# Kernel tuning notes

Hardware: AMD Instinct MI355X
Metric: run time of the kernel (lower is better)

## Reference

```python
import jax, jax.numpy as jnp
import numpy as np

D = 1024   # hidden_dim
F = 4096   # ffn_dim
E = 8      # expert_num
K = 2      # top_k
B, S = 2, 2048

def setup_inputs() -> dict:
    key = jax.random.key(0)
    ks = jax.random.split(key, 5)
    scale = 0.02
    x = jax.random.normal(ks[0], (B, S, D), dtype=jnp.float32)
    gate_w = jax.random.normal(ks[1], (D, E), dtype=jnp.float32) * scale
    w1 = jax.random.normal(ks[2], (E, D, F), dtype=jnp.float32) * scale
    w3 = jax.random.normal(ks[3], (E, D, F), dtype=jnp.float32) * scale
    w2 = jax.random.normal(ks[4], (E, F, D), dtype=jnp.float32) * scale
    return {"x": x, "gate_w": gate_w, "w1": w1, "w3": w3, "w2": w2}

def reference(x, gate_w, w1, w3, w2):
    # x: [B, S, D] -> tokens [T, D]
    Bb, Ss, Dd = x.shape
    xt = x.reshape(-1, Dd)                                  # [T, D]
    T = xt.shape[0]
    # Router: softmax over experts in float32 (matches torch dtype=torch.float)
    router_probs = jax.nn.softmax((xt @ gate_w).astype(jnp.float32), axis=-1)  # [T, E]
    topk_w, topk_idx = jax.lax.top_k(router_probs, K)        # [T, K]
    topk_w = topk_w / topk_w.sum(axis=-1, keepdims=True)
    topk_w = topk_w.astype(x.dtype)
    # Combine weights scattered to dense [T, E] (equivalent to per-expert gather/scatter loop)
    combine = jnp.zeros((T, E), dtype=x.dtype).at[jnp.arange(T)[:, None], topk_idx].add(topk_w)
    # SwishFFN per expert: w2(silu(x w1) * (x w3)), no bias
    h = jax.nn.silu(jnp.einsum('td,edf->etf', xt, w1)) * jnp.einsum('td,edf->etf', xt, w3)  # [E, T, F]
    out_e = jnp.einsum('etf,efd->etd', h, w2)                # [E, T, D]
    out = jnp.einsum('etd,te->td', out_e, combine)           # [T, D]
    return out.reshape(Bb, Ss, Dd), router_probs
```

## Files before the change

### kernel.cpp

```cpp
#include <hip/hip_runtime.h>

typedef unsigned short u16;
typedef unsigned int u32;
typedef __attribute__((ext_vector_type(8))) short bf16x8;
typedef __attribute__((ext_vector_type(4))) float f32x4;
typedef __attribute__((ext_vector_type(4))) int i32x4;
typedef __attribute__((ext_vector_type(2))) unsigned int u32x2;


__device__ __forceinline__ u16 f2bf(float f) {
  u32 u = __builtin_bit_cast(u32, f);
  u += 0x7fffu + ((u >> 16) & 1u);
  return (u16)(u >> 16);
}
__device__ __forceinline__ u32 pack2(u16 a, u16 b) { return (u32)a | ((u32)b << 16); }

__device__ __forceinline__ char* lds_swz(void* base, int row, int byteInRow) {
  return (char*)base + (((row << 7) + byteInRow) ^ ((row & 7) << 4));
}

#define GLL16(g, l) __builtin_amdgcn_global_load_lds( \
    (const __attribute__((address_space(1))) void*)(g), \
    (__attribute__((address_space(3))) void*)(l), 16, 0, 0)

__device__ __forceinline__ void wtrans256_tile(const float* __restrict__ src, u16* __restrict__ dst,
                                               int R, int C, int c0, int r0, void* lds)
{
  char* t = (char*)lds;
  const int tid = threadIdx.x;
  const int rr = (tid >> 4) * 4;
  const int cc = (tid & 15) * 4;
#pragma unroll
  for (int rp = 0; rp < 4; ++rp) {
    f32x4 v[4];
#pragma unroll
    for (int j = 0; j < 4; ++j)
      v[j] = *(const f32x4*)(src + (size_t)(r0 + rp * 64 + rr + j) * C + c0 + cc);
#pragma unroll
    for (int c = 0; c < 4; ++c) {
      u32x2 p;
      p[0] = pack2(f2bf(v[0][c]), f2bf(v[1][c]));
      p[1] = pack2(f2bf(v[2][c]), f2bf(v[3][c]));
      const int col = cc + c;
      const int rowb = (rp * 64 + rr) * 2;
      *(u32x2*)(t + col * 528 + (rowb ^ (((col >> 2) & 7) << 4))) = p;
    }
  }
  __syncthreads();
  const int c = tid >> 2;
  const int ch = (tid & 3) * 128;
  u16* dp = dst + (size_t)(c0 + c) * R + r0;
  const int sw = ((c >> 2) & 7) << 4;
#pragma unroll
  for (int k = 0; k < 8; ++k) {
    i32x4 a = *(const i32x4*)(t + c * 528 + ((ch + k * 16) ^ sw));
    *(i32x4*)((char*)dp + ch + k * 16) = a;
  }
}

__global__ __launch_bounds__(256) void prep_k(
    const float* __restrict__ w1, const float* __restrict__ w3,
    u16* __restrict__ w1t, u16* __restrict__ w3t,
    const float* __restrict__ x, const float* __restrict__ gw,
    float* __restrict__ probs, u16* __restrict__ xb,
    float* __restrict__ wa, int* __restrict__ alist, int* __restrict__ cnt)
{
  __shared__ __align__(16) char smem[33792];
  const int bid = blockIdx.x;
  if (bid >= 4096) {
    const int t0 = bid - 4096;
    const int sel = t0 >> 11;
    const int rem = t0 & 2047;
    const int e = rem >> 8;
    const int idx = rem & 255;
    const int rt = idx >> 6, ct = idx & 63;
    const float* src = (sel ? w3 : w1) + (size_t)e * 4194304;
    u16* dst = (sel ? w3t : w1t) + (size_t)e * 4194304;
    wtrans256_tile(src, dst, 1024, 4096, ct * 64, rt * 256, smem);
    return;
  }
  const int t = bid;
  const int tid = threadIdx.x;
  f32x4 xv = ((const f32x4*)(x + (size_t)t * 1024))[tid];
  u32x2 hb;
  hb[0] = pack2(f2bf(xv[0]), f2bf(xv[1]));
  hb[1] = pack2(f2bf(xv[2]), f2bf(xv[3]));
  *(u32x2*)(xb + (size_t)t * 1024 + tid * 4) = hb;

  float acc[8];
#pragma unroll
  for (int e = 0; e < 8; ++e) acc[e] = 0.f;
  const float* g = gw + tid * 32;
#pragma unroll
  for (int j = 0; j < 4; ++j)
#pragma unroll
    for (int e = 0; e < 8; ++e) acc[e] = fmaf(xv[j], g[j * 8 + e], acc[e]);

#pragma unroll
  for (int e = 0; e < 8; ++e)
    for (int off = 32; off > 0; off >>= 1) acc[e] += __shfl_down(acc[e], off);

  float* red = (float*)smem;
  const int lane = tid & 63, wid = tid >> 6;
  if (lane == 0) {
#pragma unroll
    for (int e = 0; e < 8; ++e) red[wid * 8 + e] = acc[e];
  }
  __syncthreads();
  if (tid == 0) {
    float p[8]; float mx = -1e30f;
#pragma unroll
    for (int e = 0; e < 8; ++e) { p[e] = red[e] + red[8 + e] + red[16 + e] + red[24 + e]; mx = fmaxf(mx, p[e]); }
    float s = 0.f;
#pragma unroll
    for (int e = 0; e < 8; ++e) { p[e] = __expf(p[e] - mx); s += p[e]; }
    float inv = 1.f / s;
#pragma unroll
    for (int e = 0; e < 8; ++e) { p[e] *= inv; probs[(size_t)t * 8 + e] = p[e]; }
    int i0 = 0;
#pragma unroll
    for (int e = 1; e < 8; ++e) if (p[e] > p[i0]) i0 = e;
    int i1 = (i0 == 0) ? 1 : 0;
#pragma unroll
    for (int e = 0; e < 8; ++e) if (e != i0 && p[e] > p[i1]) i1 = e;
    float s2 = p[i0] + p[i1];
    int pos0 = atomicAdd(&cnt[i0], 1); alist[i0 * 4096 + pos0] = t * 2;
    int pos1 = atomicAdd(&cnt[i1], 1); alist[i1 * 4096 + pos1] = t * 2 + 1;
    wa[t * 2]     = p[i0] / s2;
    wa[t * 2 + 1] = p[i1] / s2;
  }
}

__global__ __launch_bounds__(256, 2) void gemm1w2_k(
    const u16* __restrict__ xb, const u16* __restrict__ w1t, const u16* __restrict__ w3t,
    const int* __restrict__ alist, const int* __restrict__ cnt, u16* __restrict__ H,
    const float* __restrict__ w2, u16* __restrict__ w2t)
{
  __shared__ __align__(16) char smem[33792];
  const int e = blockIdx.z;
  const int bx = blockIdx.x;

  if (bx >= 64) {
    const int slot = (bx - 64) * 256 + blockIdx.y * 8 + e;
    const int e2 = slot >> 8;
    const int idx = slot & 255;
    const int rt = idx >> 4, ct = idx & 15;
    const float* src = w2 + (size_t)e2 * 4194304;
    u16* dst = w2t + (size_t)e2 * 4194304;
    wtrans256_tile(src, dst, 4096, 1024, ct * 64, rt * 256, smem);
    return;
  }

  u16* As = (u16*)smem;
  u16* Bs = (u16*)(smem + 16384);
  int* rowid = (int*)(smem + 32768);

  const int mc = cnt[e];
  const int m0 = blockIdx.y * 128;
  if (m0 >= mc) return;
  const int n0 = bx * 64;
  const int tid = threadIdx.x;

  if (tid < 128) rowid[tid] = (m0 + tid < mc) ? alist[e * 4096 + m0 + tid] : -1;
  __syncthreads();

  const int l = tid & 63, w = tid >> 6;
  const u16* wt = (w >> 1) ? w3t : w1t;
  u16* bbase = Bs + (w >> 1) * 4096;

  const u16* aps[4]; const u16* bps[4];
  u16* ald[4]; u16* bld[4];
#pragma unroll
  for (int q = 0; q < 4; ++q) {
    int ra = 32 * w + 8 * q + (l >> 3);
    int id = rowid[ra];
    aps[q] = xb + (size_t)(id < 0 ? 0 : (id >> 1)) * 1024 + ((l & 7) ^ (ra & 7)) * 8;
    ald[q] = As + (32 * w + 8 * q) * 64;
    int rb = 32 * (w & 1) + 8 * q + (l >> 3);
    bps[q] = wt + (size_t)e * 4194304 + (size_t)(n0 + rb) * 1024 + ((l & 7) ^ (rb & 7)) * 8;
    bld[q] = bbase + (32 * (w & 1) + 8 * q) * 64;
  }

  const int wm = (w >> 1) * 64, wn = (w & 1) * 32;
  const int l15 = l & 15, lg = l >> 4;

  f32x4 acc1[4][2], acc3[4][2];
  const f32x4 zf = {0.f, 0.f, 0.f, 0.f};
#pragma unroll
  for (int mi = 0; mi < 4; ++mi) { acc1[mi][0] = zf; acc1[mi][1] = zf; acc3[mi][0] = zf; acc3[mi][1] = zf; }

  for (int kt = 0; kt < 16; ++kt) {
    const int ko = kt * 64;
#pragma unroll
    for (int q = 0; q < 4; ++q) GLL16(aps[q] + ko, ald[q]);
#pragma unroll
    for (int q = 0; q < 4; ++q) GLL16(bps[q] + ko, bld[q]);
    __syncthreads();
#pragma unroll
    for (int ks = 0; ks < 2; ++ks) {
      const int kb = ks * 64 + lg * 16;
      bf16x8 af[4];
#pragma unroll
      for (int mi = 0; mi < 4; ++mi)
        af[mi] = *(const bf16x8*)lds_swz(As, wm + mi * 16 + l15, kb);
#pragma unroll
      for (int ni = 0; ni < 2; ++ni) {
        bf16x8 b1 = *(const bf16x8*)lds_swz(Bs, wn + ni * 16 + l15, kb);
        bf16x8 b3 = *(const bf16x8*)lds_swz(Bs + 4096, wn + ni * 16 + l15, kb);
#pragma unroll
        for (int mi = 0; mi < 4; ++mi) {
          acc1[mi][ni] = __builtin_amdgcn_mfma_f32_16x16x32_bf16(af[mi], b1, acc1[mi][ni], 0, 0, 0);
          acc3[mi][ni] = __builtin_amdgcn_mfma_f32_16x16x32_bf16(af[mi], b3, acc3[mi][ni], 0, 0, 0);
        }
      }
    }
    __syncthreads();
  }

#pragma unroll
  for (int mi = 0; mi < 4; ++mi) {
    const int rb = wm + mi * 16 + lg * 4;
#pragma unroll
    for (int ni = 0; ni < 2; ++ni) {
      const int col = n0 + wn + ni * 16 + l15;
      f32x4 c1 = acc1[mi][ni], c3 = acc3[mi][ni];
#pragma unroll
      for (int j = 0; j < 4; ++j) {
        int id = rowid[rb + j];
        if (id >= 0) {
          float a = c1[j];
          float h = (a / (1.f + __expf(-a))) * c3[j];
          H[(size_t)id * 4096 + col] = f2bf(h);
        }
      }
    }
  }
}

__global__ __launch_bounds__(256, 2) void gemm2_k(
    const u16* __restrict__ H, const u16* __restrict__ w2t,
    const int* __restrict__ alist, const int* __restrict__ cnt,
    const float* __restrict__ wa, float* __restrict__ out)
{
  const int e = blockIdx.z;
  const int mc = cnt[e];
  const int yy = blockIdx.y;
  const int kh = yy & 1;
  const int m0 = (yy >> 1) * 128;
  if (m0 >= mc) return;
  const int n0 = blockIdx.x * 128;
  const int tid = threadIdx.x;

  __shared__ u16 As[128 * 64];
  __shared__ u16 Bs[128 * 64];
  __shared__ int rowid[128];
  __shared__ float rw[128];

  if (tid < 128) {
    int id = (m0 + tid < mc) ? alist[e * 4096 + m0 + tid] : -1;
    rowid[tid] = id;
    rw[tid] = (id >= 0) ? wa[id] : 0.f;
  }
  __syncthreads();

  const int l = tid & 63, w = tid >> 6;
  const size_t kbase = (size_t)kh * 2048;
  const u16* aps[4]; const u16* bps[4];
  u16* ald[4]; u16* bld[4];
#pragma unroll
  for (int q = 0; q < 4; ++q) {
    int ra = 32 * w + 8 * q + (l >> 3);
    int id = rowid[ra];
    aps[q] = H + (size_t)(id < 0 ? 0 : id) * 4096 + kbase + ((l & 7) ^ (ra & 7)) * 8;
    ald[q] = As + (32 * w + 8 * q) * 64;
    int rb = 32 * w + 8 * q + (l >> 3);
    bps[q] = w2t + (size_t)e * 4194304 + (size_t)(n0 + rb) * 4096 + kbase + ((l & 7) ^ (rb & 7)) * 8;
    bld[q] = Bs + (32 * w + 8 * q) * 64;
  }

  const int wm = (w >> 1) * 64, wn = (w & 1) * 64;
  const int l15 = l & 15, lg = l >> 4;

  f32x4 acc[4][4];
  const f32x4 zf = {0.f, 0.f, 0.f, 0.f};
#pragma unroll
  for (int mi = 0; mi < 4; ++mi)
#pragma unroll
    for (int ni = 0; ni < 4; ++ni) acc[mi][ni] = zf;

  for (int kt = 0; kt < 32; ++kt) {
    const int ko = kt * 64;
#pragma unroll
    for (int q = 0; q < 4; ++q) GLL16(aps[q] + ko, ald[q]);
#pragma unroll
    for (int q = 0; q < 4; ++q) GLL16(bps[q] + ko, bld[q]);
    __syncthreads();
#pragma unroll
    for (int ks = 0; ks < 2; ++ks) {
      const int kb = ks * 64 + lg * 16;
      bf16x8 af[4];
#pragma unroll
      for (int mi = 0; mi < 4; ++mi)
        af[mi] = *(const bf16x8*)lds_swz(As, wm + mi * 16 + l15, kb);
#pragma unroll
      for (int ni = 0; ni < 4; ++ni) {
        bf16x8 bfb = *(const bf16x8*)lds_swz(Bs, wn + ni * 16 + l15, kb);
#pragma unroll
        for (int mi = 0; mi < 4; ++mi)
          acc[mi][ni] = __builtin_amdgcn_mfma_f32_16x16x32_bf16(af[mi], bfb, acc[mi][ni], 0, 0, 0);
      }
    }
    __syncthreads();
  }

#pragma unroll
  for (int mi = 0; mi < 4; ++mi) {
    const int rb = wm + mi * 16 + lg * 4;
#pragma unroll
    for (int ni = 0; ni < 4; ++ni) {
      const int col = n0 + wn + ni * 16 + l15;
      f32x4 c = acc[mi][ni];
#pragma unroll
      for (int j = 0; j < 4; ++j) {
        int rr = rb + j;
        int id = rowid[rr];
        if (id >= 0)
          unsafeAtomicAdd(&out[(size_t)(id >> 1) * 1024 + col], c[j] * rw[rr]);
      }
    }
  }
}

extern "C" void kernel_launch(void* const* d_in, const int* in_sizes, int n_in,
                              void* d_out, int out_size, void* d_ws, size_t ws_size,
                              hipStream_t stream)
{
  (void)in_sizes; (void)n_in; (void)out_size; (void)ws_size;
  const float* x  = (const float*)d_in[0];
  const float* gw = (const float*)d_in[1];
  const float* w1 = (const float*)d_in[2];
  const float* w3 = (const float*)d_in[3];
  const float* w2 = (const float*)d_in[4];
  float* out   = (float*)d_out;
  float* probs = out + (size_t)4096 * 1024;

  const size_t MB = (size_t)1 << 20;
  char* ws = (char*)d_ws;
  u16*   xb    = (u16*)(ws);
  u16*   H     = (u16*)(ws + 8 * MB);
  u16*   w1t   = (u16*)(ws + 72 * MB);
  u16*   w3t   = (u16*)(ws + 136 * MB);
  u16*   w2t   = (u16*)(ws + 200 * MB);
  float* wa    = (float*)(ws + 264 * MB);
  int*   alist = (int*)(ws + 264 * MB + 32768);
  int*   cnt   = (int*)(ws + 264 * MB + 32768 + 131072);

  hipMemsetAsync(cnt, 0, 8 * sizeof(int), stream);
  hipMemsetAsync(out, 0, (size_t)4096 * 1024 * sizeof(float), stream);
  prep_k<<<8192, 256, 0, stream>>>(w1, w3, w1t, w3t, x, gw, probs, xb, wa, alist, cnt);
  gemm1w2_k<<<dim3(72, 32, 8), 256, 0, stream>>>(xb, w1t, w3t, alist, cnt, H, w2, w2t);
  gemm2_k<<<dim3(8, 64, 8), 256, 0, stream>>>(H, w2t, alist, cnt, wa, out);
}
```

Before: 510.7 us.

## Pipeline weight transpose with double-buffered async global-to-LDS loads

Replaces the per-tile register-staged fp32-to-bf16 weight transpose with a loop that streams several 64-row tiles per block. Each tile is loaded with global_load_lds into one half of a double-buffered LDS region while the other half is converted and written out. The w1/w3 transpose now covers 512 rows per block, so the prep grid shrinks, and the w2 transpose is also remapped. The goal is to overlap load latency with conversion in this bandwidth-bound prep step. In exchange there are more barriers, and the LDS reads now run without the previous bank-conflict swizzle.

```diff
diff --git a/kernel.cpp b/kernel.cpp
--- a/kernel.cpp
+++ b/kernel.cpp
@@ -23,38 +23,44 @@
     (const __attribute__((address_space(1))) void*)(g), \
     (__attribute__((address_space(3))) void*)(l), 16, 0, 0)
 
-__device__ __forceinline__ void wtrans256_tile(const float* __restrict__ src, u16* __restrict__ dst,
-                                               int R, int C, int c0, int r0, void* lds)
-{
-  char* t = (char*)lds;
+__device__ __forceinline__ void trans_tiles(
+    const float* __restrict__ src, u16* __restrict__ dst,
+    int Cs, int Rs, int c0, int r0base, int NT, float* lds )
+{
   const int tid = threadIdx.x;
-  const int rr = (tid >> 4) * 4;
-  const int cc = (tid & 15) * 4;
-#pragma unroll
-  for (int rp = 0; rp < 4; ++rp) {
-    f32x4 v[4];
-#pragma unroll
-    for (int j = 0; j < 4; ++j)
-      v[j] = *(const f32x4*)(src + (size_t)(r0 + rp * 64 + rr + j) * C + c0 + cc);
-#pragma unroll
-    for (int c = 0; c < 4; ++c) {
-      u32x2 p;
-      p[0] = pack2(f2bf(v[0][c]), f2bf(v[1][c]));
-      p[1] = pack2(f2bf(v[2][c]), f2bf(v[3][c]));
-      const int col = cc + c;
-      const int rowb = (rp * 64 + rr) * 2;
-      *(u32x2*)(t + col * 528 + (rowb ^ (((col >> 2) & 7) << 4))) = p;
-    }
-  }
-  __syncthreads();
-  const int c = tid >> 2;
-  const int ch = (tid & 3) * 128;
-  u16* dp = dst + (size_t)(c0 + c) * R + r0;
-  const int sw = ((c >> 2) & 7) << 4;
-#pragma unroll
-  for (int k = 0; k < 8; ++k) {
-    i32x4 a = *(const i32x4*)(t + c * 528 + ((ch + k * 16) ^ sw));
-    *(i32x4*)((char*)dp + ch + k * 16) = a;
+  const int w = tid >> 6, l = tid & 63;
+  const float* sbase = src + (size_t)(r0base + w * 16 + (l >> 4)) * Cs + c0 + (l & 15) * 4;
+  const int c = tid & 63, rseg = tid >> 6;
+
+#pragma unroll
+  for (int q = 0; q < 4; ++q)
+    GLL16(sbase + (size_t)(q * 4) * Cs, lds + (w * 16 + q * 4) * 64);
+
+  for (int t = 0; t < NT; ++t) {
+    if (t + 1 < NT) {
+      const float* sb2 = sbase + (size_t)((t + 1) * 64) * Cs;
+      float* lb2 = lds + ((t + 1) & 1) * 4096;
+#pragma unroll
+      for (int q = 0; q < 4; ++q)
+        GLL16(sb2 + (size_t)(q * 4) * Cs, lb2 + (w * 16 + q * 4) * 64);
+      asm volatile("s_waitcnt vmcnt(4)" ::: "memory");
+    } else {
+      asm volatile("s_waitcnt vmcnt(0)" ::: "memory");
+    }
+    __builtin_amdgcn_s_barrier();
+    const float* tb = lds + (t & 1) * 4096;
+    u32 p[8];
+#pragma unroll
+    for (int i = 0; i < 8; ++i) {
+      float a  = tb[(rseg * 16 + 2 * i) * 64 + c];
+      float bv = tb[(rseg * 16 + 2 * i + 1) * 64 + c];
+      p[i] = pack2(f2bf(a), f2bf(bv));
+    }
+    u16* dp = dst + (size_t)(c0 + c) * Rs + r0base + t * 64 + rseg * 16;
+    *(i32x4*)dp = *(i32x4*)&p[0];
+    *(i32x4*)(dp + 8) = *(i32x4*)&p[4];
+    asm volatile("s_waitcnt lgkmcnt(0)" ::: "memory");
+    __builtin_amdgcn_s_barrier();
   }
 }
 
@@ -65,18 +71,19 @@
     float* __restrict__ probs, u16* __restrict__ xb,
     float* __restrict__ wa, int* __restrict__ alist, int* __restrict__ cnt)
 {
-  __shared__ __align__(16) char smem[33792];
+  __shared__ __align__(16) float smem[2][4096];
   const int bid = blockIdx.x;
   if (bid >= 4096) {
     const int t0 = bid - 4096;
-    const int sel = t0 >> 11;
-    const int rem = t0 & 2047;
-    const int e = rem >> 8;
-    const int idx = rem & 255;
-    const int rt = idx >> 6, ct = idx & 63;
+    const int sel = t0 >> 10;
+    const int rem = t0 & 1023;
+    const int e = rem >> 7;
+    const int rem2 = rem & 127;
+    const int ct = rem2 >> 1;
+    const int rh = rem2 & 1;
     const float* src = (sel ? w3 : w1) + (size_t)e * 4194304;
     u16* dst = (sel ? w3t : w1t) + (size_t)e * 4194304;
-    wtrans256_tile(src, dst, 1024, 4096, ct * 64, rt * 256, smem);
+    trans_tiles(src, dst, 4096, 1024, ct * 64, rh * 512, 8, &smem[0][0]);
     return;
   }
   const int t = bid;
@@ -100,7 +107,7 @@
   for (int e = 0; e < 8; ++e)
     for (int off = 32; off > 0; off >>= 1) acc[e] += __shfl_down(acc[e], off);
 
-  float* red = (float*)smem;
+  float* red = &smem[0][0];
   const int lane = tid & 63, wid = tid >> 6;
   if (lane == 0) {
 #pragma unroll
@@ -136,7 +143,7 @@
     const int* __restrict__ alist, const int* __restrict__ cnt, u16* __restrict__ H,
     const float* __restrict__ w2, u16* __restrict__ w2t)
 {
-  __shared__ __align__(16) char smem[33792];
+  __shared__ __align__(16) char smem[33280];
   const int e = blockIdx.z;
   const int bx = blockIdx.x;
 
@@ -144,10 +151,9 @@
     const int slot = (bx - 64) * 256 + blockIdx.y * 8 + e;
     const int e2 = slot >> 8;
     const int idx = slot & 255;
-    const int rt = idx >> 4, ct = idx & 15;
     const float* src = w2 + (size_t)e2 * 4194304;
     u16* dst = w2t + (size_t)e2 * 4194304;
-    wtrans256_tile(src, dst, 4096, 1024, ct * 64, rt * 256, smem);
+    trans_tiles(src, dst, 1024, 4096, (idx >> 4) * 64, (idx & 15) * 256, 4, (float*)smem);
     return;
   }
 
@@ -357,7 +363,7 @@
 
   hipMemsetAsync(cnt, 0, 8 * sizeof(int), stream);
   hipMemsetAsync(out, 0, (size_t)4096 * 1024 * sizeof(float), stream);
-  prep_k<<<8192, 256, 0, stream>>>(w1, w3, w1t, w3t, x, gw, probs, xb, wa, alist, cnt);
+  prep_k<<<6144, 256, 0, stream>>>(w1, w3, w1t, w3t, x, gw, probs, xb, wa, alist, cnt);
   gemm1w2_k<<<dim3(72, 32, 8), 256, 0, stream>>>(xb, w1t, w3t, alist, cnt, H, w2, w2t);
   gemm2_k<<<dim3(8, 64, 8), 256, 0, stream>>>(H, w2t, alist, cnt, wa, out);
 }
```

Result: no change. 510.5 us (-0.0%).

## Store transposed weights in tile-contiguous blocked layout loaded via LDS DMA

Applied to the files above, without the earlier changes.

Replaces the row-major transpose of w1/w3/w2 into bf16 with a blocked layout in which each 64-row by 64-k tile sits contiguously in memory. The GEMM B-operand loads then walk contiguous 8KB blocks instead of strided rows. The transpose kernels now stage fp32 input with global_load_lds and write packed bf16 rows directly. The w2 transpose grid grows, which adds extra blocks to gemm1w2, and the change depends on the new index math being correct.

```diff
diff --git a/kernel.cpp b/kernel.cpp
--- a/kernel.cpp
+++ b/kernel.cpp
@@ -23,64 +23,49 @@
     (const __attribute__((address_space(1))) void*)(g), \
     (__attribute__((address_space(3))) void*)(l), 16, 0, 0)
 
-__device__ __forceinline__ void wtrans256_tile(const float* __restrict__ src, u16* __restrict__ dst,
-                                               int R, int C, int c0, int r0, void* lds)
-{
-  char* t = (char*)lds;
-  const int tid = threadIdx.x;
-  const int rr = (tid >> 4) * 4;
-  const int cc = (tid & 15) * 4;
-#pragma unroll
-  for (int rp = 0; rp < 4; ++rp) {
-    f32x4 v[4];
-#pragma unroll
-    for (int j = 0; j < 4; ++j)
-      v[j] = *(const f32x4*)(src + (size_t)(r0 + rp * 64 + rr + j) * C + c0 + cc);
-#pragma unroll
-    for (int c = 0; c < 4; ++c) {
-      u32x2 p;
-      p[0] = pack2(f2bf(v[0][c]), f2bf(v[1][c]));
-      p[1] = pack2(f2bf(v[2][c]), f2bf(v[3][c]));
-      const int col = cc + c;
-      const int rowb = (rp * 64 + rr) * 2;
-      *(u32x2*)(t + col * 528 + (rowb ^ (((col >> 2) & 7) << 4))) = p;
-    }
-  }
-  __syncthreads();
-  const int c = tid >> 2;
-  const int ch = (tid & 3) * 128;
-  u16* dp = dst + (size_t)(c0 + c) * R + r0;
-  const int sw = ((c >> 2) & 7) << 4;
-#pragma unroll
-  for (int k = 0; k < 8; ++k) {
-    i32x4 a = *(const i32x4*)(t + c * 528 + ((ch + k * 16) ^ sw));
-    *(i32x4*)((char*)dp + ch + k * 16) = a;
-  }
-}
-
-__global__ __launch_bounds__(256) void prep_k(
+__global__ __launch_bounds__(256) void prep13_k(
     const float* __restrict__ w1, const float* __restrict__ w3,
     u16* __restrict__ w1t, u16* __restrict__ w3t,
     const float* __restrict__ x, const float* __restrict__ gw,
     float* __restrict__ probs, u16* __restrict__ xb,
     float* __restrict__ wa, int* __restrict__ alist, int* __restrict__ cnt)
 {
-  __shared__ __align__(16) char smem[33792];
+  __shared__ __align__(16) float smem[16384];
   const int bid = blockIdx.x;
+  const int tid = threadIdx.x;
   if (bid >= 4096) {
     const int t0 = bid - 4096;
     const int sel = t0 >> 11;
-    const int rem = t0 & 2047;
-    const int e = rem >> 8;
-    const int idx = rem & 255;
-    const int rt = idx >> 6, ct = idx & 63;
-    const float* src = (sel ? w3 : w1) + (size_t)e * 4194304;
-    u16* dst = (sel ? w3t : w1t) + (size_t)e * 4194304;
-    wtrans256_tile(src, dst, 1024, 4096, ct * 64, rt * 256, smem);
+    const int e   = (t0 >> 8) & 7;
+    const int ktb = (t0 >> 4) & 15;
+    const int nc  = t0 & 15;
+    const float* src = (sel ? w3 : w1) + (size_t)e * 4194304 + (size_t)(ktb * 64) * 4096 + nc * 256;
+    u16* dstb = (sel ? w3t : w1t) + (size_t)e * 64 * 16 * 4096 + (size_t)ktb * 4096;
+
+    const int w = tid >> 6, l = tid & 63;
+#pragma unroll
+    for (int q = 0; q < 16; ++q) {
+      const int r = w * 16 + q;
+      GLL16(src + (size_t)r * 4096 + l * 4, smem + r * 256);
+    }
+    asm volatile("s_waitcnt vmcnt(0)" ::: "memory");
+    __syncthreads();
+
+    u32 p[32];
+#pragma unroll
+    for (int i = 0; i < 32; ++i) {
+      float a = smem[(2 * i) * 256 + tid];
+      float b = smem[(2 * i + 1) * 256 + tid];
+      p[i] = pack2(f2bf(a), f2bf(b));
+    }
+    const int s = tid >> 6, n = tid & 63;
+    u16* dp = dstb + (size_t)(nc * 4 + s) * 16 * 4096 + n * 64;
+#pragma unroll
+    for (int k = 0; k < 8; ++k)
+      *(i32x4*)(dp + k * 8) = *(const i32x4*)&p[k * 4];
     return;
   }
   const int t = bid;
-  const int tid = threadIdx.x;
   f32x4 xv = ((const f32x4*)(x + (size_t)t * 1024))[tid];
   u32x2 hb;
   hb[0] = pack2(f2bf(xv[0]), f2bf(xv[1]));
@@ -100,7 +85,7 @@
   for (int e = 0; e < 8; ++e)
     for (int off = 32; off > 0; off >>= 1) acc[e] += __shfl_down(acc[e], off);
 
-  float* red = (float*)smem;
+  float* red = smem;
   const int lane = tid & 63, wid = tid >> 6;
   if (lane == 0) {
 #pragma unroll
@@ -136,18 +121,41 @@
     const int* __restrict__ alist, const int* __restrict__ cnt, u16* __restrict__ H,
     const float* __restrict__ w2, u16* __restrict__ w2t)
 {
-  __shared__ __align__(16) char smem[33792];
+  __shared__ __align__(16) char smem[33280];
   const int e = blockIdx.z;
   const int bx = blockIdx.x;
+  const int tid = threadIdx.x;
 
   if (bx >= 64) {
-    const int slot = (bx - 64) * 256 + blockIdx.y * 8 + e;
-    const int e2 = slot >> 8;
-    const int idx = slot & 255;
-    const int rt = idx >> 4, ct = idx & 15;
-    const float* src = w2 + (size_t)e2 * 4194304;
-    u16* dst = w2t + (size_t)e2 * 4194304;
-    wtrans256_tile(src, dst, 4096, 1024, ct * 64, rt * 256, smem);
+    const int slot = ((bx - 64) * 32 + blockIdx.y) * 8 + e;
+    const int e2  = slot >> 9;
+    const int ktb = (slot >> 3) & 63;
+    const int nc  = slot & 7;
+    const float* src = w2 + (size_t)e2 * 4194304 + (size_t)(ktb * 64) * 1024 + nc * 128;
+    float* lds = (float*)smem;
+
+    const int w = tid >> 6, l = tid & 63;
+#pragma unroll
+    for (int q = 0; q < 8; ++q) {
+      const int r2 = w * 8 + q;
+      GLL16(src + (size_t)(2 * r2 + (l >> 5)) * 1024 + (l & 31) * 4, lds + r2 * 256);
+    }
+    asm volatile("s_waitcnt vmcnt(0)" ::: "memory");
+    __syncthreads();
+
+    const int s = (tid >> 6) & 1, n = tid & 63, kh2 = tid >> 7;
+    const int cc = s * 64 + n;
+    u32 p[16];
+#pragma unroll
+    for (int i = 0; i < 16; ++i) {
+      float a = lds[(kh2 * 32 + 2 * i) * 128 + cc];
+      float b = lds[(kh2 * 32 + 2 * i + 1) * 128 + cc];
+      p[i] = pack2(f2bf(a), f2bf(b));
+    }
+    u16* dp = w2t + (((size_t)e2 * 16 + nc * 2 + s) * 64 + ktb) * 4096 + n * 64 + kh2 * 32;
+#pragma unroll
+    for (int k = 0; k < 4; ++k)
+      *(i32x4*)(dp + k * 8) = *(const i32x4*)&p[k * 4];
     return;
   }
 
@@ -159,7 +167,6 @@
   const int m0 = blockIdx.y * 128;
   if (m0 >= mc) return;
   const int n0 = bx * 64;
-  const int tid = threadIdx.x;
 
   if (tid < 128) rowid[tid] = (m0 + tid < mc) ? alist[e * 4096 + m0 + tid] : -1;
   __syncthreads();
@@ -177,7 +184,7 @@
     aps[q] = xb + (size_t)(id < 0 ? 0 : (id >> 1)) * 1024 + ((l & 7) ^ (ra & 7)) * 8;
     ald[q] = As + (32 * w + 8 * q) * 64;
     int rb = 32 * (w & 1) + 8 * q + (l >> 3);
-    bps[q] = wt + (size_t)e * 4194304 + (size_t)(n0 + rb) * 1024 + ((l & 7) ^ (rb & 7)) * 8;
+    bps[q] = wt + ((size_t)e * 64 + bx) * 16 * 4096 + rb * 64 + ((l & 7) ^ (rb & 7)) * 8;
     bld[q] = bbase + (32 * (w & 1) + 8 * q) * 64;
   }
 
@@ -190,11 +197,10 @@
   for (int mi = 0; mi < 4; ++mi) { acc1[mi][0] = zf; acc1[mi][1] = zf; acc3[mi][0] = zf; acc3[mi][1] = zf; }
 
   for (int kt = 0; kt < 16; ++kt) {
-    const int ko = kt * 64;
-#pragma unroll
-    for (int q = 0; q < 4; ++q) GLL16(aps[q] + ko, ald[q]);
-#pragma unroll
-    for (int q = 0; q < 4; ++q) GLL16(bps[q] + ko, bld[q]);
+#pragma unroll
+    for (int q = 0; q < 4; ++q) GLL16(aps[q] + kt * 64, ald[q]);
+#pragma unroll
+    for (int q = 0; q < 4; ++q) GLL16(bps[q] + kt * 4096, bld[q]);
     __syncthreads();
 #pragma unroll
     for (int ks = 0; ks < 2; ++ks) {
@@ -274,7 +280,8 @@
     aps[q] = H + (size_t)(id < 0 ? 0 : id) * 4096 + kbase + ((l & 7) ^ (ra & 7)) * 8;
     ald[q] = As + (32 * w + 8 * q) * 64;
     int rb = 32 * w + 8 * q + (l >> 3);
-    bps[q] = w2t + (size_t)e * 4194304 + (size_t)(n0 + rb) * 4096 + kbase + ((l & 7) ^ (rb & 7)) * 8;
+    int nt = (n0 >> 6) + (rb >> 6);
+    bps[q] = w2t + (((size_t)e * 16 + nt) * 64 + kh * 32) * 4096 + (rb & 63) * 64 + ((l & 7) ^ (rb & 7)) * 8;
     bld[q] = Bs + (32 * w + 8 * q) * 64;
   }
 
@@ -289,11 +296,10 @@
     for (int ni = 0; ni < 4; ++ni) acc[mi][ni] = zf;
 
   for (int kt = 0; kt < 32; ++kt) {
-    const int ko = kt * 64;
-#pragma unroll
-    for (int q = 0; q < 4; ++q) GLL16(aps[q] + ko, ald[q]);
-#pragma unroll
-    for (int q = 0; q < 4; ++q) GLL16(bps[q] + ko, bld[q]);
+#pragma unroll
+    for (int q = 0; q < 4; ++q) GLL16(aps[q] + kt * 64, ald[q]);
+#pragma unroll
+    for (int q = 0; q < 4; ++q) GLL16(bps[q] + kt * 4096, bld[q]);
     __syncthreads();
 #pragma unroll
     for (int ks = 0; ks < 2; ++ks) {
@@ -357,7 +363,7 @@
 
   hipMemsetAsync(cnt, 0, 8 * sizeof(int), stream);
   hipMemsetAsync(out, 0, (size_t)4096 * 1024 * sizeof(float), stream);
-  prep_k<<<8192, 256, 0, stream>>>(w1, w3, w1t, w3t, x, gw, probs, xb, wa, alist, cnt);
-  gemm1w2_k<<<dim3(72, 32, 8), 256, 0, stream>>>(xb, w1t, w3t, alist, cnt, H, w2, w2t);
+  prep13_k<<<8192, 256, 0, stream>>>(w1, w3, w1t, w3t, x, gw, probs, xb, wa, alist, cnt);
+  gemm1w2_k<<<dim3(80, 32, 8), 256, 0, stream>>>(xb, w1t, w3t, alist, cnt, H, w2, w2t);
   gemm2_k<<<dim3(8, 64, 8), 256, 0, stream>>>(H, w2t, alist, cnt, wa, out);
 }
```

After: 500.9 us. No clear change (-1.9%).

## Split expert pipeline so weight transposes overlap with grouped GEMM1 work

Applied to the files above, without the earlier changes.

The prep kernel now transposes w1/w3 only for experts 0-3. Experts 4-7 are transposed inside a new kernel that runs GEMM1 for experts 0-3, and the w2 transpose rides along with GEMM1 for experts 4-7. The goal is to hide weight-conversion bandwidth behind the MFMA work instead of front-loading it before any GEMM starts. It adds a kernel launch and relies on the stream ordering the l2a transpose before l2b reads w1t/w3t for experts 4-7.

```diff
diff --git a/kernel.cpp b/kernel.cpp
--- a/kernel.cpp
+++ b/kernel.cpp
@@ -58,7 +58,7 @@
   }
 }
 
-__global__ __launch_bounds__(256) void prep_k(
+__global__ __launch_bounds__(256) void l1_k(
     const float* __restrict__ w1, const float* __restrict__ w3,
     u16* __restrict__ w1t, u16* __restrict__ w3t,
     const float* __restrict__ x, const float* __restrict__ gw,
@@ -69,8 +69,8 @@
   const int bid = blockIdx.x;
   if (bid >= 4096) {
     const int t0 = bid - 4096;
-    const int sel = t0 >> 11;
-    const int rem = t0 & 2047;
+    const int sel = t0 >> 10;
+    const int rem = t0 & 1023;
     const int e = rem >> 8;
     const int idx = rem & 255;
     const int rt = idx >> 6, ct = idx & 63;
@@ -131,26 +131,10 @@
   }
 }
 
-__global__ __launch_bounds__(256, 2) void gemm1w2_k(
-    const u16* __restrict__ xb, const u16* __restrict__ w1t, const u16* __restrict__ w3t,
-    const int* __restrict__ alist, const int* __restrict__ cnt, u16* __restrict__ H,
-    const float* __restrict__ w2, u16* __restrict__ w2t)
-{
-  __shared__ __align__(16) char smem[33792];
-  const int e = blockIdx.z;
-  const int bx = blockIdx.x;
-
-  if (bx >= 64) {
-    const int slot = (bx - 64) * 256 + blockIdx.y * 8 + e;
-    const int e2 = slot >> 8;
-    const int idx = slot & 255;
-    const int rt = idx >> 4, ct = idx & 15;
-    const float* src = w2 + (size_t)e2 * 4194304;
-    u16* dst = w2t + (size_t)e2 * 4194304;
-    wtrans256_tile(src, dst, 4096, 1024, ct * 64, rt * 256, smem);
-    return;
-  }
-
+__device__ __forceinline__ void gemm1_body(
+    char* smem, const u16* __restrict__ xb, const u16* __restrict__ w1t, const u16* __restrict__ w3t,
+    const int* __restrict__ alist, const int* __restrict__ cnt, u16* __restrict__ H, int e)
+{
   u16* As = (u16*)smem;
   u16* Bs = (u16*)(smem + 16384);
   int* rowid = (int*)(smem + 32768);
@@ -158,7 +142,7 @@
   const int mc = cnt[e];
   const int m0 = blockIdx.y * 128;
   if (m0 >= mc) return;
-  const int n0 = bx * 64;
+  const int n0 = blockIdx.x * 64;
   const int tid = threadIdx.x;
 
   if (tid < 128) rowid[tid] = (m0 + tid < mc) ? alist[e * 4096 + m0 + tid] : -1;
@@ -222,7 +206,7 @@
     const int rb = wm + mi * 16 + lg * 4;
 #pragma unroll
     for (int ni = 0; ni < 2; ++ni) {
-      const int col = n0 + wn + ni * 16 + l15;
+      const int col = blockIdx.x * 64 + wn + ni * 16 + l15;
       f32x4 c1 = acc1[mi][ni], c3 = acc3[mi][ni];
 #pragma unroll
       for (int j = 0; j < 4; ++j) {
@@ -235,6 +219,49 @@
       }
     }
   }
+}
+
+__global__ __launch_bounds__(256, 2) void l2a_k(
+    const u16* __restrict__ xb, const u16* __restrict__ w1t, const u16* __restrict__ w3t,
+    const int* __restrict__ alist, const int* __restrict__ cnt, u16* __restrict__ H,
+    const float* __restrict__ w1, const float* __restrict__ w3,
+    u16* __restrict__ w1to, u16* __restrict__ w3to)
+{
+  __shared__ __align__(16) char smem[33792];
+  const int bx = blockIdx.x;
+  if (bx >= 64) {
+    const int slot = ((bx - 64) * 32 + blockIdx.y) * 4 + blockIdx.z;
+    const int sel = slot >> 10;
+    const int r = slot & 1023;
+    const int e2 = 4 + (r >> 8);
+    const int idx = r & 255;
+    const int rt = idx >> 6, ct = idx & 63;
+    const float* src = (sel ? w3 : w1) + (size_t)e2 * 4194304;
+    u16* dst = (sel ? w3to : w1to) + (size_t)e2 * 4194304;
+    wtrans256_tile(src, dst, 1024, 4096, ct * 64, rt * 256, smem);
+    return;
+  }
+  gemm1_body(smem, xb, w1t, w3t, alist, cnt, H, blockIdx.z);
+}
+
+__global__ __launch_bounds__(256, 2) void l2b_k(
+    const u16* __restrict__ xb, const u16* __restrict__ w1t, const u16* __restrict__ w3t,
+    const int* __restrict__ alist, const int* __restrict__ cnt, u16* __restrict__ H,
+    const float* __restrict__ w2, u16* __restrict__ w2t)
+{
+  __shared__ __align__(16) char smem[33792];
+  const int bx = blockIdx.x;
+  if (bx >= 64) {
+    const int slot = ((bx - 64) * 32 + blockIdx.y) * 4 + blockIdx.z;
+    const int e2 = slot >> 8;
+    const int idx = slot & 255;
+    const int rt = idx >> 4, ct = idx & 15;
+    const float* src = w2 + (size_t)e2 * 4194304;
+    u16* dst = w2t + (size_t)e2 * 4194304;
+    wtrans256_tile(src, dst, 4096, 1024, ct * 64, rt * 256, smem);
+    return;
+  }
+  gemm1_body(smem, xb, w1t, w3t, alist, cnt, H, blockIdx.z + 4);
 }
 
 __global__ __launch_bounds__(256, 2) void gemm2_k(
@@ -355,9 +382,10 @@
   int*   alist = (int*)(ws + 264 * MB + 32768);
   int*   cnt   = (int*)(ws + 264 * MB + 32768 + 131072);
 
-  hipMemsetAsync(cnt, 0, 8 * sizeof(int), stream);
-  hipMemsetAsync(out, 0, (size_t)4096 * 1024 * sizeof(float), stream);
-  prep_k<<<8192, 256, 0, stream>>>(w1, w3, w1t, w3t, x, gw, probs, xb, wa, alist, cnt);
-  gemm1w2_k<<<dim3(72, 32, 8), 256, 0, stream>>>(xb, w1t, w3t, alist, cnt, H, w2, w2t);
+  (void)hipMemsetAsync(cnt, 0, 8 * sizeof(int), stream);
+  (void)hipMemsetAsync(out, 0, (size_t)4096 * 1024 * sizeof(float), stream);
+  l1_k<<<6144, 256, 0, stream>>>(w1, w3, w1t, w3t, x, gw, probs, xb, wa, alist, cnt);
+  l2a_k<<<dim3(80, 32, 4), 256, 0, stream>>>(xb, w1t, w3t, alist, cnt, H, w1, w3, w1t, w3t);
+  l2b_k<<<dim3(80, 32, 4), 256, 0, stream>>>(xb, w1t, w3t, alist, cnt, H, w2, w2t);
   gemm2_k<<<dim3(8, 64, 8), 256, 0, stream>>>(H, w2t, alist, cnt, wa, out);
 }
```

Measured after the change: 513.9 us. About the same (+0.6%).
